# Kernel tuning notes

Measured on AMD Instinct MI355X. Metric: run time of the kernel, lower is better.

The kernel has to match this reference:

```python
import jax, jax.numpy as jnp
import numpy as np

V = 5023          # FLAME vertex count
NJ = 5            # joints: global, neck, jaw, eyeL, eyeR
N_SHAPE = 100
N_EXP = 50
PARENTS = np.array([-1, 0, 1, 1, 1], dtype=np.int64)  # static kintree
N_BATCH = 2048


def setup_inputs() -> dict:
    key = jax.random.key(0)
    ks = jax.random.split(key, 12)
    N = N_BATCH
    shape = jax.random.normal(ks[0], (N, N_SHAPE), jnp.float32)
    exp = jax.random.normal(ks[1], (N, N_EXP), jnp.float32)
    neck_pose = 0.1 * jax.random.normal(ks[2], (N, 3), jnp.float32)
    jaw_pose = 0.1 * jax.random.normal(ks[3], (N, 3), jnp.float32)
    eye_pose = 0.1 * jax.random.normal(ks[4], (N, 6), jnp.float32)
    v_template = jax.random.normal(ks[5], (V, 3), jnp.float32)
    shapedirs = 0.01 * jax.random.normal(ks[6], (V, 3, N_SHAPE + N_EXP), jnp.float32)
    posedirs = 0.01 * jax.random.normal(ks[7], (36, V * 3), jnp.float32)
    J_regressor = jax.random.uniform(ks[8], (NJ, V), jnp.float32)
    J_regressor = J_regressor / J_regressor.sum(axis=1, keepdims=True)
    lbs_weights = jax.random.uniform(ks[9], (V, NJ), jnp.float32)
    lbs_weights = lbs_weights / lbs_weights.sum(axis=1, keepdims=True)
    parents = jnp.asarray(PARENTS)
    return dict(shape=shape, exp=exp, neck_pose=neck_pose, jaw_pose=jaw_pose,
                eye_pose=eye_pose, v_template=v_template, shapedirs=shapedirs,
                posedirs=posedirs, J_regressor=J_regressor, lbs_weights=lbs_weights,
                parents=parents)


def rodrigues(rot_vecs):
    """Axis-angle [...,3] -> rotation matrices [...,3,3] (matches SMPL/FLAME impl)."""
    angle = jnp.linalg.norm(rot_vecs + 1e-8, axis=-1, keepdims=True)
    rd = rot_vecs / angle
    cos = jnp.cos(angle)[..., None]
    sin = jnp.sin(angle)[..., None]
    rx, ry, rz = rd[..., 0], rd[..., 1], rd[..., 2]
    z = jnp.zeros_like(rx)
    K = jnp.stack([z, -rz, ry, rz, z, -rx, -ry, rx, z], axis=-1).reshape(rd.shape + (3,))
    I = jnp.eye(3, dtype=rot_vecs.dtype)
    return I + sin * K + (1.0 - cos) * (K @ K)


def flame_forward(shape, exp, neck_pose, jaw_pose, eye_pose, v_template,
                  shapedirs, posedirs, J_regressor, lbs_weights):
    N = shape.shape[0]
    dt = shape.dtype
    betas = jnp.concatenate([shape, exp], axis=1)                      # [N,150]
    # full pose: zeroed global rot + neck + jaw + eyes -> [N,NJ,3]
    full_pose = jnp.concatenate([jnp.zeros_like(jaw_pose), neck_pose,
                                 jaw_pose, eye_pose], axis=1).reshape(N, NJ, 3)
    # shape blendshapes
    v_shaped = v_template[None] + jnp.einsum('bl,vkl->bvk', betas, shapedirs)  # [N,V,3]
    J = jnp.einsum('jv,bvk->bjk', J_regressor, v_shaped)               # [N,NJ,3]
    # pose blendshapes
    R = rodrigues(full_pose)                                           # [N,NJ,3,3]
    pose_feature = (R[:, 1:] - jnp.eye(3, dtype=dt)).reshape(N, (NJ - 1) * 9)
    v_posed = v_shaped + (pose_feature @ posedirs).reshape(N, V, 3)
    # kinematic chain (static 5-joint tree)
    rel_J = J.at[:, 1:].add(-J[:, PARENTS[1:]])
    Rt = jnp.concatenate([R, rel_J[..., None]], axis=-1)               # [N,NJ,3,4]
    bottom = jnp.broadcast_to(jnp.array([0., 0., 0., 1.], dtype=dt), (N, NJ, 1, 4))
    T = jnp.concatenate([Rt, bottom], axis=2)                          # [N,NJ,4,4]
    chain = [T[:, 0]]
    for i in range(1, NJ):
        chain.append(chain[int(PARENTS[i])] @ T[:, i])
    G = jnp.stack(chain, axis=1)                                       # [N,NJ,4,4]
    # remove rest-pose joint locations from the transforms
    J_h = jnp.concatenate([J, jnp.zeros((N, NJ, 1), dt)], axis=-1)     # [N,NJ,4]
    t_corr = jnp.einsum('bjrc,bjc->bjr', G, J_h)
    A = G.at[..., 3].add(-t_corr)                                      # [N,NJ,4,4]
    # linear blend skinning
    Tw = jnp.einsum('vj,bjrc->bvrc', lbs_weights, A)                   # [N,V,4,4]
    v_h = jnp.concatenate([v_posed, jnp.ones((N, V, 1), dt)], axis=-1)
    verts = jnp.einsum('bvrc,bvc->bvr', Tw, v_h)[..., :3]              # [N,V,3]
    return verts


def reference(shape, exp, neck_pose, jaw_pose, eye_pose, v_template,
              shapedirs, posedirs, J_regressor, lbs_weights, parents):
    # parents is a static buffer (PARENTS) -- accepted for signature parity.
    return flame_forward(shape, exp, neck_pose, jaw_pose, eye_pose, v_template,
                         shapedirs, posedirs, J_regressor, lbs_weights)
```

## Files before the change

kernel.cpp:

```cpp
#include <hip/hip_runtime.h>
#include <hip/hip_bf16.h>
#include <math.h>

#define NV   5023
#define N3   15069
#define NB   2048
#define NTIL 79
#define NPAD (NTIL*192)

#define WS_JD_B   0
#define WS_ATR_B  9216
#define WS_PF_B   500736
#define WS_AB_B   795648
#define WS_BB_B   1582080

typedef __attribute__((ext_vector_type(8))) short short8;
typedef __attribute__((ext_vector_type(4))) float floatx4;

__global__ void k_zero(char* ws) {
    int i = blockIdx.x * 256 + threadIdx.x;
    if (i < 2272) ((float*)(ws + WS_JD_B))[i] = 0.f;
}

__global__ void k_jdirs(const float* __restrict__ Jreg,
                        const float* __restrict__ sdirs,
                        const float* __restrict__ vt,
                        char* __restrict__ ws) {
    int slice = blockIdx.x;
    int start = slice * 40;
    int end   = min(start + 40, NV);
    int t = threadIdx.x;
    int s0 = t, s1 = t + 256;
    float a0[5] = {0,0,0,0,0}, a1[5] = {0,0,0,0,0};
    for (int v = start; v < end; ++v) {
        float w[5];
        #pragma unroll
        for (int j = 0; j < 5; ++j) w[j] = Jreg[j * NV + v];
        float x0 = (s0 < 450) ? sdirs[(size_t)v * 450 + s0]
                 : (s0 < 453 ? vt[v * 3 + (s0 - 450)] : 0.f);
        float x1 = (s1 < 450) ? sdirs[(size_t)v * 450 + s1]
                 : (s1 < 453 ? vt[v * 3 + (s1 - 450)] : 0.f);
        #pragma unroll
        for (int j = 0; j < 5; ++j) { a0[j] += w[j] * x0; a1[j] += w[j] * x1; }
    }
    float* Jd = (float*)(ws + WS_JD_B);
    #pragma unroll
    for (int j = 0; j < 5; ++j) {
        if (s0 < 453) atomicAdd(&Jd[j * 453 + s0], a0[j]);
        if (s1 < 453) atomicAdd(&Jd[j * 453 + s1], a1[j]);
    }
}

__global__ void k_batch(const float* __restrict__ shp,
                        const float* __restrict__ expn,
                        const float* __restrict__ neck,
                        const float* __restrict__ jaw,
                        const float* __restrict__ eye,
                        char* __restrict__ ws) {
    __shared__ float JdL[2265];
    {
        const float* Jd = (const float*)(ws + WS_JD_B);
        for (int i = threadIdx.x; i < 2265; i += 256) JdL[i] = Jd[i];
    }
    __syncthreads();
    int b = blockIdx.x * 256 + threadIdx.x;
    float* pf  = (float*)(ws + WS_PF_B) + (size_t)b * 36;
    float* Atr = (float*)(ws + WS_ATR_B) + (size_t)b * 60;

    float J[15];
    for (int jk = 0; jk < 15; ++jk) J[jk] = JdL[(jk / 3) * 453 + 450 + (jk % 3)];
    for (int l = 0; l < 150; ++l) {
        float be = (l < 100) ? shp[(size_t)b * 100 + l] : expn[(size_t)b * 50 + (l - 100)];
        #pragma unroll
        for (int jj = 0; jj < 5; ++jj)
            #pragma unroll
            for (int kk = 0; kk < 3; ++kk)
                J[jj * 3 + kk] += JdL[jj * 453 + kk * 150 + l] * be;
    }

    float R[5][9];
    for (int jj = 0; jj < 5; ++jj) {
        float rx, ry, rz;
        if (jj == 0)      { rx = 0.f; ry = 0.f; rz = 0.f; }
        else if (jj == 1) { rx = neck[b*3]; ry = neck[b*3+1]; rz = neck[b*3+2]; }
        else if (jj == 2) { rx = jaw[b*3];  ry = jaw[b*3+1];  rz = jaw[b*3+2];  }
        else if (jj == 3) { rx = eye[b*6];  ry = eye[b*6+1];  rz = eye[b*6+2];  }
        else              { rx = eye[b*6+3]; ry = eye[b*6+4]; rz = eye[b*6+5];  }
        float ax = rx + 1e-8f, ay = ry + 1e-8f, az = rz + 1e-8f;
        float angle = sqrtf(ax*ax + ay*ay + az*az);
        float inv = 1.f / angle;
        float ux = rx * inv, uy = ry * inv, uz = rz * inv;
        float c = cosf(angle), s = sinf(angle);
        float K[9] = {0.f, -uz, uy,  uz, 0.f, -ux,  -uy, ux, 0.f};
        float KK[9];
        #pragma unroll
        for (int r = 0; r < 3; ++r)
            #pragma unroll
            for (int cc = 0; cc < 3; ++cc) {
                float a = 0.f;
                #pragma unroll
                for (int m = 0; m < 3; ++m) a += K[r*3+m] * K[m*3+cc];
                KK[r*3+cc] = a;
            }
        #pragma unroll
        for (int e = 0; e < 9; ++e) R[jj][e] = s * K[e] + (1.f - c) * KK[e];
        R[jj][0] += 1.f; R[jj][4] += 1.f; R[jj][8] += 1.f;
    }

    for (int jj = 1; jj < 5; ++jj)
        #pragma unroll
        for (int e = 0; e < 9; ++e)
            pf[(jj-1)*9 + e] = R[jj][e] - ((e == 0 || e == 4 || e == 8) ? 1.f : 0.f);

    float G[5][12];
    #pragma unroll
    for (int r = 0; r < 3; ++r) {
        #pragma unroll
        for (int cc = 0; cc < 3; ++cc) G[0][r*4+cc] = R[0][r*3+cc];
        G[0][r*4+3] = J[r];
    }
    const int par[5] = {-1, 0, 1, 1, 1};
    for (int jj = 1; jj < 5; ++jj) {
        int p = par[jj];
        float rel[3];
        #pragma unroll
        for (int r = 0; r < 3; ++r) rel[r] = J[jj*3+r] - J[p*3+r];
        #pragma unroll
        for (int r = 0; r < 3; ++r) {
            #pragma unroll
            for (int cc = 0; cc < 3; ++cc) {
                float a = 0.f;
                #pragma unroll
                for (int m = 0; m < 3; ++m) a += G[p][r*4+m] * R[jj][m*3+cc];
                G[jj][r*4+cc] = a;
            }
            float tt = G[p][r*4+3];
            #pragma unroll
            for (int m = 0; m < 3; ++m) tt += G[p][r*4+m] * rel[m];
            G[jj][r*4+3] = tt;
        }
    }
    for (int jj = 0; jj < 5; ++jj)
        #pragma unroll
        for (int r = 0; r < 3; ++r) {
            float tc = 0.f;
            #pragma unroll
            for (int m = 0; m < 3; ++m) tc += G[jj][r*4+m] * J[jj*3+m];
            Atr[jj*12 + r*4 + 0] = G[jj][r*4+0];
            Atr[jj*12 + r*4 + 1] = G[jj][r*4+1];
            Atr[jj*12 + r*4 + 2] = G[jj][r*4+2];
            Atr[jj*12 + r*4 + 3] = G[jj][r*4+3] - tc;
        }
}

__global__ void k_aconv(const float* __restrict__ shp,
                        const float* __restrict__ expn,
                        char* __restrict__ ws) {
    int idx = blockIdx.x * 256 + threadIdx.x;
    int b = idx / 192, k = idx % 192;
    float v;
    if (k < 100)      v = shp[(size_t)b * 100 + k];
    else if (k < 150) v = expn[(size_t)b * 50 + (k - 100)];
    else if (k < 186) v = ((const float*)(ws + WS_PF_B))[(size_t)b * 36 + (k - 150)];
    else              v = 0.f;
    ((__hip_bfloat16*)(ws + WS_AB_B))[idx] = __float2bfloat16(v);
}

__global__ void k_bconv(const float* __restrict__ sdirs,
                        const float* __restrict__ pdirs,
                        char* __restrict__ ws) {
    int idx = blockIdx.x * 256 + threadIdx.x;
    int kg = idx % 24, n = idx / 24;
    int k0 = kg * 8;
    __hip_bfloat16 val[8];
    #pragma unroll
    for (int e = 0; e < 8; ++e) {
        int k = k0 + e;
        float v = 0.f;
        if (n < N3) {
            if (k < 150)      v = sdirs[(size_t)n * 150 + k];
            else if (k < 186) v = pdirs[(size_t)(k - 150) * N3 + n];
        }
        val[e] = __float2bfloat16(v);
    }
    *(int4*)((__hip_bfloat16*)(ws + WS_BB_B) + (size_t)n * 192 + k0) = *(int4*)val;
}

#define A_OFF  0
#define B_OFF  17408
#define S_VT   65
#define S_AT   61
#define VT_T_OFF 0
#define ATR_OFF  49920
#define VTQ_OFF  65536
#define LBS_OFF  66304
#define SMEM_BYTES 67584

__global__ __launch_bounds__(256, 2) void k_mega(
        const char* __restrict__ ws,
        const float* __restrict__ vt,
        const float* __restrict__ lbsw,
        float* __restrict__ out) {
    __shared__ __align__(16) unsigned char smem[SMEM_BYTES];
    const unsigned char* AbG = (const unsigned char*)ws + WS_AB_B;
    const unsigned char* BbG = (const unsigned char*)ws + WS_BB_B;
    const float* AtrG = (const float*)(ws + WS_ATR_B);

    const int ntile = blockIdx.y;
    const int b0    = blockIdx.x * 128;
    const int t     = threadIdx.x;
    const int lane  = t & 63;
    const int wn    = t >> 6;
    const int l15 = lane & 15, quad = lane >> 4;

    floatx4 acc[8][3];
    #pragma unroll
    for (int f = 0; f < 8; ++f)
        #pragma unroll
        for (int g = 0; g < 3; ++g) {
            floatx4 z = {0.f, 0.f, 0.f, 0.f};
            acc[f][g] = z;
        }

    for (int chunk = 0; chunk < 3; ++chunk) {
        __syncthreads();
        #pragma unroll
        for (int i = 0; i < 4; ++i) {
            int flat = i * 256 + t;
            int row = flat >> 3, piece = flat & 7;
            *(float4*)(smem + A_OFF + row * 136 + piece * 16) =
                *(const float4*)(AbG + (size_t)(b0 + row) * 384 + chunk * 128 + piece * 16);
        }
        #pragma unroll
        for (int i = 0; i < 6; ++i) {
            int flat = i * 256 + t;
            int row = flat >> 3, piece = flat & 7;
            *(float4*)(smem + B_OFF + row * 136 + piece * 16) =
                *(const float4*)(BbG + (size_t)(ntile * 192 + row) * 384 + chunk * 128 + piece * 16);
        }
        __syncthreads();
        #pragma unroll
        for (int ks = 0; ks < 2; ++ks) {
            short8 af[8];
            #pragma unroll
            for (int f = 0; f < 8; ++f)
                af[f] = *(const short8*)(smem + A_OFF + (f * 16 + l15) * 136 + ks * 64 + quad * 16);
            #pragma unroll
            for (int g = 0; g < 3; ++g) {
                short8 bf = *(const short8*)(smem + B_OFF + (wn * 48 + g * 16 + l15) * 136 + ks * 64 + quad * 16);
                #pragma unroll
                for (int f = 0; f < 8; ++f)
                    acc[f][g] = __builtin_amdgcn_mfma_f32_16x16x32_bf16(af[f], bf, acc[f][g], 0, 0, 0);
            }
        }
    }
    __syncthreads();

    float* vtT  = (float*)(smem + VT_T_OFF);
    float* atrS = (float*)(smem + ATR_OFF);
    float* vtQ  = (float*)(smem + VTQ_OFF);
    float* lbsS = (float*)(smem + LBS_OFF);

    if (t < 192) { int n = ntile * 192 + t; vtQ[t] = (n < N3) ? vt[n] : 0.f; }
    for (int i = t; i < 320; i += 256) {
        int v = ntile * 64 + i / 5;
        lbsS[i] = (v < NV) ? lbsw[(size_t)v * 5 + (i % 5)] : 0.f;
    }

    #pragma unroll
    for (int half = 0; half < 2; ++half) {
        __syncthreads();
        #pragma unroll
        for (int ff = 0; ff < 4; ++ff) {
            int f = half * 4 + ff;
            #pragma unroll
            for (int g = 0; g < 3; ++g) {
                int col = wn * 48 + g * 16 + l15;
                int rl  = ff * 16 + quad * 4;
                #pragma unroll
                for (int r = 0; r < 4; ++r)
                    vtT[col * S_VT + rl + r] = acc[f][g][r];
            }
        }
        for (int i = t; i < 3840; i += 256) {
            int rw = i / 60, cw = i - rw * 60;
            atrS[rw * S_AT + cw] = AtrG[((size_t)b0 + half * 64) * 60 + i];
        }
        __syncthreads();

        {
            int rl = t & 63;
            int vgrp = t >> 6;
            float ar[60];
            #pragma unroll
            for (int i = 0; i < 60; ++i) ar[i] = atrS[rl * S_AT + i];
            for (int vv = 0; vv < 16; ++vv) {
                int vloc = vgrp * 16 + vv;
                int c0 = vloc * 3;
                float w0 = lbsS[vloc*5+0], w1 = lbsS[vloc*5+1], w2 = lbsS[vloc*5+2],
                      w3 = lbsS[vloc*5+3], w4 = lbsS[vloc*5+4];
                float px = vtT[(c0+0) * S_VT + rl] + vtQ[c0+0];
                float py = vtT[(c0+1) * S_VT + rl] + vtQ[c0+1];
                float pz = vtT[(c0+2) * S_VT + rl] + vtQ[c0+2];
                float y[3];
                #pragma unroll
                for (int r = 0; r < 3; ++r) {
                    float t0 = w0*ar[ 0+r*4+0] + w1*ar[12+r*4+0] + w2*ar[24+r*4+0]
                             + w3*ar[36+r*4+0] + w4*ar[48+r*4+0];
                    float t1 = w0*ar[ 0+r*4+1] + w1*ar[12+r*4+1] + w2*ar[24+r*4+1]
                             + w3*ar[36+r*4+1] + w4*ar[48+r*4+1];
                    float t2 = w0*ar[ 0+r*4+2] + w1*ar[12+r*4+2] + w2*ar[24+r*4+2]
                             + w3*ar[36+r*4+2] + w4*ar[48+r*4+2];
                    float t3 = w0*ar[ 0+r*4+3] + w1*ar[12+r*4+3] + w2*ar[24+r*4+3]
                             + w3*ar[36+r*4+3] + w4*ar[48+r*4+3];
                    y[r] = t0*px + t1*py + t2*pz + t3;
                }
                vtT[(c0+0) * S_VT + rl] = y[0];
                vtT[(c0+1) * S_VT + rl] = y[1];
                vtT[(c0+2) * S_VT + rl] = y[2];
            }
        }
        __syncthreads();
        {
            int wv = t >> 6;
            const bool full = (ntile * 192 + 192 <= N3);
            for (int rr = wv; rr < 64; rr += 4) {
                size_t ob = (size_t)(b0 + half * 64 + rr) * N3 + (size_t)ntile * 192;
                if (full) {
                    #pragma unroll
                    for (int e = 0; e < 3; ++e) {
                        int col = e * 64 + lane;
                        __builtin_nontemporal_store(vtT[col * S_VT + rr], &out[ob + col]);
                    }
                } else {
                    #pragma unroll
                    for (int e = 0; e < 3; ++e) {
                        int col = e * 64 + lane;
                        if (ntile * 192 + col < N3)
                            __builtin_nontemporal_store(vtT[col * S_VT + rr], &out[ob + col]);
                    }
                }
            }
        }
    }
}

extern "C" void kernel_launch(void* const* d_in, const int* in_sizes, int n_in,
                              void* d_out, int out_size, void* d_ws, size_t ws_size,
                              hipStream_t stream) {
    const float* shp  = (const float*)d_in[0];
    const float* expn = (const float*)d_in[1];
    const float* neck = (const float*)d_in[2];
    const float* jaw  = (const float*)d_in[3];
    const float* eye  = (const float*)d_in[4];
    const float* vt   = (const float*)d_in[5];
    const float* sdir = (const float*)d_in[6];
    const float* pdir = (const float*)d_in[7];
    const float* jreg = (const float*)d_in[8];
    const float* lbsw = (const float*)d_in[9];
    char* ws  = (char*)d_ws;
    float* out = (float*)d_out;

    k_zero <<<9,   256, 0, stream>>>(ws);
    k_jdirs<<<126, 256, 0, stream>>>(jreg, sdir, vt, ws);
    k_batch<<<8,   256, 0, stream>>>(shp, expn, neck, jaw, eye, ws);
    k_aconv<<<1536, 256, 0, stream>>>(shp, expn, ws);
    k_bconv<<<1422, 256, 0, stream>>>(sdir, pdir, ws);
    k_mega <<<dim3(16, NTIL), 256, 0, stream>>>(ws, vt, lbsw, out);
}
```

Baseline: 295.3 us.

## Fuse prep kernels, pack A operand in k_batch, shrink mega epilogue smem for occupancy

Merges the joint-regressor reduction and the B-operand bf16 conversion into one launch, and drops the separate A-conversion kernel by having k_batch write bf16-packed betas and pose features directly, with vectorized loads and more, smaller blocks. The k_mega epilogue now processes 32-row quarters instead of 64-row halves. This cuts LDS use so launch bounds can target 3 blocks per CU, and the barriers are replaced with explicit lgkmcnt waits. This removes two launches and an fp32 round trip through the workspace, at the cost of more barrier rounds in the epilogue and tighter register limits.

Measured after the change: 281.6 us. 1.05x faster.

```diff
diff --git a/kernel.cpp b/kernel.cpp
--- a/kernel.cpp
+++ b/kernel.cpp
@@ -10,44 +10,77 @@
 
 #define WS_JD_B   0
 #define WS_ATR_B  9216
-#define WS_PF_B   500736
 #define WS_AB_B   795648
 #define WS_BB_B   1582080
 
 typedef __attribute__((ext_vector_type(8))) short short8;
 typedef __attribute__((ext_vector_type(4))) float floatx4;
+
+static __device__ __forceinline__ unsigned short f2bf(float x) {
+    union { __hip_bfloat16 h; unsigned short s; } u;
+    u.h = __float2bfloat16(x);
+    return u.s;
+}
+static __device__ __forceinline__ unsigned int pk2(float a, float b) {
+    return (unsigned int)f2bf(a) | ((unsigned int)f2bf(b) << 16);
+}
+
+#define BAR_LGKM() do { \
+    asm volatile("s_waitcnt lgkmcnt(0)" ::: "memory"); \
+    __builtin_amdgcn_s_barrier(); \
+    asm volatile("" ::: "memory"); \
+} while (0)
 
 __global__ void k_zero(char* ws) {
     int i = blockIdx.x * 256 + threadIdx.x;
     if (i < 2272) ((float*)(ws + WS_JD_B))[i] = 0.f;
 }
 
-__global__ void k_jdirs(const float* __restrict__ Jreg,
-                        const float* __restrict__ sdirs,
-                        const float* __restrict__ vt,
-                        char* __restrict__ ws) {
-    int slice = blockIdx.x;
-    int start = slice * 40;
-    int end   = min(start + 40, NV);
-    int t = threadIdx.x;
-    int s0 = t, s1 = t + 256;
-    float a0[5] = {0,0,0,0,0}, a1[5] = {0,0,0,0,0};
-    for (int v = start; v < end; ++v) {
-        float w[5];
-        #pragma unroll
-        for (int j = 0; j < 5; ++j) w[j] = Jreg[j * NV + v];
-        float x0 = (s0 < 450) ? sdirs[(size_t)v * 450 + s0]
-                 : (s0 < 453 ? vt[v * 3 + (s0 - 450)] : 0.f);
-        float x1 = (s1 < 450) ? sdirs[(size_t)v * 450 + s1]
-                 : (s1 < 453 ? vt[v * 3 + (s1 - 450)] : 0.f);
-        #pragma unroll
-        for (int j = 0; j < 5; ++j) { a0[j] += w[j] * x0; a1[j] += w[j] * x1; }
-    }
-    float* Jd = (float*)(ws + WS_JD_B);
-    #pragma unroll
-    for (int j = 0; j < 5; ++j) {
-        if (s0 < 453) atomicAdd(&Jd[j * 453 + s0], a0[j]);
-        if (s1 < 453) atomicAdd(&Jd[j * 453 + s1], a1[j]);
+__global__ void k_prep(const float* __restrict__ Jreg,
+                       const float* __restrict__ sdirs,
+                       const float* __restrict__ vt,
+                       const float* __restrict__ pdirs,
+                       char* __restrict__ ws) {
+    if (blockIdx.x < 126) {
+        int slice = blockIdx.x;
+        int start = slice * 40;
+        int end   = min(start + 40, NV);
+        int t = threadIdx.x;
+        int s0 = t, s1 = t + 256;
+        float a0[5] = {0,0,0,0,0}, a1[5] = {0,0,0,0,0};
+        for (int v = start; v < end; ++v) {
+            float w[5];
+            #pragma unroll
+            for (int j = 0; j < 5; ++j) w[j] = Jreg[j * NV + v];
+            float x0 = (s0 < 450) ? sdirs[(size_t)v * 450 + s0]
+                     : (s0 < 453 ? vt[v * 3 + (s0 - 450)] : 0.f);
+            float x1 = (s1 < 450) ? sdirs[(size_t)v * 450 + s1]
+                     : (s1 < 453 ? vt[v * 3 + (s1 - 450)] : 0.f);
+            #pragma unroll
+            for (int j = 0; j < 5; ++j) { a0[j] += w[j] * x0; a1[j] += w[j] * x1; }
+        }
+        float* Jd = (float*)(ws + WS_JD_B);
+        #pragma unroll
+        for (int j = 0; j < 5; ++j) {
+            if (s0 < 453) atomicAdd(&Jd[j * 453 + s0], a0[j]);
+            if (s1 < 453) atomicAdd(&Jd[j * 453 + s1], a1[j]);
+        }
+    } else {
+        int idx = (blockIdx.x - 126) * 256 + threadIdx.x;
+        int kg = idx % 24, n = idx / 24;
+        int k0 = kg * 8;
+        __hip_bfloat16 val[8];
+        #pragma unroll
+        for (int e = 0; e < 8; ++e) {
+            int k = k0 + e;
+            float v = 0.f;
+            if (n < N3) {
+                if (k < 150)      v = sdirs[(size_t)n * 150 + k];
+                else if (k < 186) v = pdirs[(size_t)(k - 150) * N3 + n];
+            }
+            val[e] = __float2bfloat16(v);
+        }
+        *(int4*)((__hip_bfloat16*)(ws + WS_BB_B) + (size_t)n * 192 + k0) = *(int4*)val;
     }
 }
 
@@ -60,22 +93,45 @@
     __shared__ float JdL[2265];
     {
         const float* Jd = (const float*)(ws + WS_JD_B);
-        for (int i = threadIdx.x; i < 2265; i += 256) JdL[i] = Jd[i];
+        for (int i = threadIdx.x; i < 2265; i += 64) JdL[i] = Jd[i];
     }
     __syncthreads();
-    int b = blockIdx.x * 256 + threadIdx.x;
-    float* pf  = (float*)(ws + WS_PF_B) + (size_t)b * 36;
+    int b = blockIdx.x * 64 + threadIdx.x;
     float* Atr = (float*)(ws + WS_ATR_B) + (size_t)b * 60;
+    unsigned int* A32 = (unsigned int*)((char*)ws + WS_AB_B + (size_t)b * 384);
 
     float J[15];
+    #pragma unroll
     for (int jk = 0; jk < 15; ++jk) J[jk] = JdL[(jk / 3) * 453 + 450 + (jk % 3)];
-    for (int l = 0; l < 150; ++l) {
-        float be = (l < 100) ? shp[(size_t)b * 100 + l] : expn[(size_t)b * 50 + (l - 100)];
-        #pragma unroll
-        for (int jj = 0; jj < 5; ++jj)
-            #pragma unroll
-            for (int kk = 0; kk < 3; ++kk)
-                J[jj * 3 + kk] += JdL[jj * 453 + kk * 150 + l] * be;
+
+    for (int l4 = 0; l4 < 25; ++l4) {
+        float4 be = *(const float4*)(shp + (size_t)b * 100 + l4 * 4);
+        A32[2*l4]     = pk2(be.x, be.y);
+        A32[2*l4 + 1] = pk2(be.z, be.w);
+        float bev[4] = {be.x, be.y, be.z, be.w};
+        #pragma unroll
+        for (int e = 0; e < 4; ++e) {
+            int l = l4 * 4 + e;
+            #pragma unroll
+            for (int jj = 0; jj < 5; ++jj)
+                #pragma unroll
+                for (int kk = 0; kk < 3; ++kk)
+                    J[jj * 3 + kk] += JdL[jj * 453 + kk * 150 + l] * bev[e];
+        }
+    }
+    for (int l2 = 0; l2 < 25; ++l2) {
+        float2 be = *(const float2*)(expn + (size_t)b * 50 + l2 * 2);
+        A32[50 + l2] = pk2(be.x, be.y);
+        float bev[2] = {be.x, be.y};
+        #pragma unroll
+        for (int e = 0; e < 2; ++e) {
+            int l = 100 + l2 * 2 + e;
+            #pragma unroll
+            for (int jj = 0; jj < 5; ++jj)
+                #pragma unroll
+                for (int kk = 0; kk < 3; ++kk)
+                    J[jj * 3 + kk] += JdL[jj * 453 + kk * 150 + l] * bev[e];
+        }
     }
 
     float R[5][9];
@@ -107,10 +163,15 @@
         R[jj][0] += 1.f; R[jj][4] += 1.f; R[jj][8] += 1.f;
     }
 
+    float pf_loc[36];
+    #pragma unroll
     for (int jj = 1; jj < 5; ++jj)
         #pragma unroll
         for (int e = 0; e < 9; ++e)
-            pf[(jj-1)*9 + e] = R[jj][e] - ((e == 0 || e == 4 || e == 8) ? 1.f : 0.f);
+            pf_loc[(jj-1)*9 + e] = R[jj][e] - ((e == 0 || e == 4 || e == 8) ? 1.f : 0.f);
+    #pragma unroll
+    for (int i = 0; i < 18; ++i) A32[75 + i] = pk2(pf_loc[2*i], pf_loc[2*i + 1]);
+    A32[93] = 0u; A32[94] = 0u; A32[95] = 0u;
 
     float G[5][12];
     #pragma unroll
@@ -153,50 +214,17 @@
         }
 }
 
-__global__ void k_aconv(const float* __restrict__ shp,
-                        const float* __restrict__ expn,
-                        char* __restrict__ ws) {
-    int idx = blockIdx.x * 256 + threadIdx.x;
-    int b = idx / 192, k = idx % 192;
-    float v;
-    if (k < 100)      v = shp[(size_t)b * 100 + k];
-    else if (k < 150) v = expn[(size_t)b * 50 + (k - 100)];
-    else if (k < 186) v = ((const float*)(ws + WS_PF_B))[(size_t)b * 36 + (k - 150)];
-    else              v = 0.f;
-    ((__hip_bfloat16*)(ws + WS_AB_B))[idx] = __float2bfloat16(v);
-}
-
-__global__ void k_bconv(const float* __restrict__ sdirs,
-                        const float* __restrict__ pdirs,
-                        char* __restrict__ ws) {
-    int idx = blockIdx.x * 256 + threadIdx.x;
-    int kg = idx % 24, n = idx / 24;
-    int k0 = kg * 8;
-    __hip_bfloat16 val[8];
-    #pragma unroll
-    for (int e = 0; e < 8; ++e) {
-        int k = k0 + e;
-        float v = 0.f;
-        if (n < N3) {
-            if (k < 150)      v = sdirs[(size_t)n * 150 + k];
-            else if (k < 186) v = pdirs[(size_t)(k - 150) * N3 + n];
-        }
-        val[e] = __float2bfloat16(v);
-    }
-    *(int4*)((__hip_bfloat16*)(ws + WS_BB_B) + (size_t)n * 192 + k0) = *(int4*)val;
-}
-
 #define A_OFF  0
 #define B_OFF  17408
-#define S_VT   65
+#define S_VT   33
 #define S_AT   61
 #define VT_T_OFF 0
-#define ATR_OFF  49920
-#define VTQ_OFF  65536
-#define LBS_OFF  66304
-#define SMEM_BYTES 67584
-
-__global__ __launch_bounds__(256, 2) void k_mega(
+#define ATR_OFF  25344
+#define VTQ_OFF  33152
+#define LBS_OFF  33920
+#define SMEM_BYTES 43520
+
+__global__ __launch_bounds__(256, 3) void k_mega(
         const char* __restrict__ ws,
         const float* __restrict__ vt,
         const float* __restrict__ lbsw,
@@ -268,34 +296,35 @@
     }
 
     #pragma unroll
-    for (int half = 0; half < 2; ++half) {
-        __syncthreads();
-        #pragma unroll
-        for (int ff = 0; ff < 4; ++ff) {
-            int f = half * 4 + ff;
+    for (int q = 0; q < 4; ++q) {
+        BAR_LGKM();
+        #pragma unroll
+        for (int ff2 = 0; ff2 < 2; ++ff2) {
+            int f = q * 2 + ff2;
             #pragma unroll
             for (int g = 0; g < 3; ++g) {
                 int col = wn * 48 + g * 16 + l15;
-                int rl  = ff * 16 + quad * 4;
+                int rl  = ff2 * 16 + quad * 4;
                 #pragma unroll
                 for (int r = 0; r < 4; ++r)
                     vtT[col * S_VT + rl + r] = acc[f][g][r];
             }
         }
-        for (int i = t; i < 3840; i += 256) {
+        for (int i = t; i < 1920; i += 256) {
             int rw = i / 60, cw = i - rw * 60;
-            atrS[rw * S_AT + cw] = AtrG[((size_t)b0 + half * 64) * 60 + i];
-        }
-        __syncthreads();
+            atrS[rw * S_AT + cw] = AtrG[((size_t)(b0 + q * 32)) * 60 + i];
+        }
+        BAR_LGKM();
 
         {
-            int rl = t & 63;
-            int vgrp = t >> 6;
+            int rl = t & 31;
+            int vgrp = t >> 5;
             float ar[60];
             #pragma unroll
             for (int i = 0; i < 60; ++i) ar[i] = atrS[rl * S_AT + i];
-            for (int vv = 0; vv < 16; ++vv) {
-                int vloc = vgrp * 16 + vv;
+            #pragma unroll
+            for (int vv = 0; vv < 8; ++vv) {
+                int vloc = vgrp * 8 + vv;
                 int c0 = vloc * 3;
                 float w0 = lbsS[vloc*5+0], w1 = lbsS[vloc*5+1], w2 = lbsS[vloc*5+2],
                       w3 = lbsS[vloc*5+3], w4 = lbsS[vloc*5+4];
@@ -320,12 +349,12 @@
                 vtT[(c0+2) * S_VT + rl] = y[2];
             }
         }
-        __syncthreads();
+        BAR_LGKM();
         {
             int wv = t >> 6;
             const bool full = (ntile * 192 + 192 <= N3);
-            for (int rr = wv; rr < 64; rr += 4) {
-                size_t ob = (size_t)(b0 + half * 64 + rr) * N3 + (size_t)ntile * 192;
+            for (int rr = wv; rr < 32; rr += 4) {
+                size_t ob = (size_t)(b0 + q * 32 + rr) * N3 + (size_t)ntile * 192;
                 if (full) {
                     #pragma unroll
                     for (int e = 0; e < 3; ++e) {
@@ -361,10 +390,8 @@
     char* ws  = (char*)d_ws;
     float* out = (float*)d_out;
 
-    k_zero <<<9,   256, 0, stream>>>(ws);
-    k_jdirs<<<126, 256, 0, stream>>>(jreg, sdir, vt, ws);
-    k_batch<<<8,   256, 0, stream>>>(shp, expn, neck, jaw, eye, ws);
-    k_aconv<<<1536, 256, 0, stream>>>(shp, expn, ws);
-    k_bconv<<<1422, 256, 0, stream>>>(sdir, pdir, ws);
+    k_zero <<<9,    256, 0, stream>>>(ws);
+    k_prep <<<1548, 256, 0, stream>>>(jreg, sdir, vt, pdir, ws);
+    k_batch<<<32,    64, 0, stream>>>(shp, expn, neck, jaw, eye, ws);
     k_mega <<<dim3(16, NTIL), 256, 0, stream>>>(ws, vt, lbsw, out);
 }
```
